# Optimization experiments

Hardware: AMD Instinct MI355X
Metric: run time of the kernel (lower is better)

## Reference

```python
import math
import jax, jax.numpy as jnp
import numpy as np

B, TP, E, H, HKV, D, M = 4, 8192, 4096, 32, 8, 128, 256
OUTLIERS = 8  # outlier_count_general
ROPE_THETA = 10000.0


def rotate_half(x):
    h = x.shape[-1] // 2
    return jnp.concatenate([-x[..., h:], x[..., :h]], axis=-1)


def setup_inputs() -> dict:
    key = jax.random.key(0)
    ks = jax.random.split(key, 9)
    hidden_states = jax.random.normal(ks[0], (B, 1, E), jnp.float32)
    # rotary embedding for the single new token at position TP
    inv_freq = 1.0 / (ROPE_THETA ** (np.arange(0, D, 2, dtype=np.float32) / D))
    ang = np.float32(TP) * inv_freq  # [D/2]
    cos = jnp.broadcast_to(jnp.asarray(np.concatenate([np.cos(ang), np.cos(ang)]), jnp.float32)[None, None, :], (B, 1, D))
    sin = jnp.broadcast_to(jnp.asarray(np.concatenate([np.sin(ang), np.sin(ang)]), jnp.float32)[None, None, :], (B, 1, D))
    past_keys = jax.random.normal(ks[1], (B, HKV, TP, D), jnp.float32)
    past_values = jax.random.normal(ks[2], (B, HKV, TP, D), jnp.float32)
    attention_mask = jnp.ones((B, TP + 1), jnp.float32)
    sc = E ** -0.5
    Wq = jax.random.normal(ks[3], (H * D, E), jnp.float32) * sc
    Wk = jax.random.normal(ks[4], (HKV * D, E), jnp.float32) * sc
    Wv = jax.random.normal(ks[5], (HKV * D, E), jnp.float32) * sc
    Wo = jax.random.normal(ks[6], (E, H * D), jnp.float32) * sc
    S_proj = jax.random.normal(ks[7], (D, M), jnp.float32)  # JL sketch matrix, shared across heads
    return {"hidden_states": hidden_states, "cos": cos, "sin": sin,
            "past_keys": past_keys, "past_values": past_values,
            "attention_mask": attention_mask,
            "Wq": Wq, "Wk": Wk, "Wv": Wv, "Wo": Wo, "S_proj": S_proj}


def reference(hidden_states, cos, sin, past_keys, past_values, attention_mask, Wq, Wk, Wv, Wo, S_proj):
    b = hidden_states.shape[0]
    d = past_keys.shape[-1]
    hkv = past_keys.shape[1]
    h = Wq.shape[0] // d
    g = h // hkv  # num_key_value_groups
    m = S_proj.shape[-1]

    # projections (decode step, q_len == 1)
    q = (hidden_states @ Wq.T).reshape(b, 1, h, d).transpose(0, 2, 1, 3)    # [b,H,1,d]
    k = (hidden_states @ Wk.T).reshape(b, 1, hkv, d).transpose(0, 2, 1, 3)  # [b,Hkv,1,d]
    v = (hidden_states @ Wv.T).reshape(b, 1, hkv, d).transpose(0, 2, 1, 3)

    # rotary
    c = cos[:, None, :, :]  # [b,1,1,d]
    s = sin[:, None, :, :]
    q = q * c + rotate_half(q) * s
    k = k * c + rotate_half(k) * s

    # update_sketch: append new key; keys held as raw values, quantized below
    keys = jnp.concatenate([past_keys, k], axis=2)      # [b,Hkv,T,d]
    values = jnp.concatenate([past_values, v], axis=2)  # [b,Hkv,T,d]

    # outlier channels: top-|.| channels per (batch, kv-head) kept exact
    ch_score = jnp.mean(jnp.abs(keys), axis=2)          # [b,Hkv,d]
    _, idx = jax.lax.top_k(ch_score, OUTLIERS)
    omask = jnp.sum(jax.nn.one_hot(idx, d, dtype=keys.dtype), axis=-2)  # [b,Hkv,d] in {0,1}

    # QJL 1-bit quantization of inlier part: store sign(S^T k_in) and ||k_in||
    k_in = keys * (1.0 - omask)[:, :, None, :]
    norms = jnp.linalg.norm(k_in, axis=-1)              # [b,Hkv,T]
    signs = jnp.sign(jnp.einsum('bktd,dm->bktm', k_in, S_proj))  # [b,Hkv,T,m]

    # attention_score: unbiased estimator q.k ~ ||k|| * sqrt(pi/2)/m * <S q, sign(S k)>
    qg = q[:, :, 0, :].reshape(b, hkv, g, d)            # group queries by kv head
    q_in = qg * (1.0 - omask)[:, :, None, :]
    q_out = qg * omask[:, :, None, :]
    qs = jnp.einsum('bkgd,dm->bkgm', q_in, S_proj)
    est = jnp.einsum('bkgm,bktm->bkgt', qs, signs) * (math.sqrt(math.pi / 2.0) / m) * norms[:, :, None, :]
    exact = jnp.einsum('bkgd,bktd->bkgt', q_out, keys)  # outlier channels kept full precision
    attn = (est + exact) / math.sqrt(d)                 # [b,Hkv,G,T]

    attn = attn + (1.0 - attention_mask)[:, None, None, :] * jnp.finfo(attn.dtype).min
    w = jax.nn.softmax(attn, axis=-1)

    out = jnp.einsum('bkgt,bktd->bkgd', w, values).reshape(b, 1, h * d)
    return out @ Wo.T  # [b,1,E]
```

## Files before the change

kernel.cpp:

```cpp
#include <hip/hip_runtime.h>
#include <math.h>

#define BB 4
#define TP 8192
#define TT 8193
#define EE 4096
#define HH 32
#define HKV 8
#define DD 128
#define MM 256
#define GG 4
#define NSEG 48
#define ESPLIT 4
#define TB 64
#define NT2 129
#define WCH 65

#define CJL 0.0048957583420918762f
#define RSQRT_D 0.08838834764831845f
#define NEG_HUGE -3.402823466e38f

#define KSTR 136
#define SSTR 276

typedef _Float16 f16x8 __attribute__((ext_vector_type(8)));
typedef _Float16 f16x4 __attribute__((ext_vector_type(4)));
typedef float f32x4 __attribute__((ext_vector_type(4)));

#define OFF_Q      0
#define OFF_KN     16384
#define OFF_VN     20480
#define OFF_MASKF  24576
#define OFF_QOV    28672
#define OFF_AO     29696
#define OFF_INT    46080
#define OFF_QSF    50432
#define OFF_SFRAG  115968
#define OFF_QKVP   181504
#define OFF_SCOREP 279808
#define OFF_LOGITS 541952

__global__ __launch_bounds__(256) void k1_kernel(
    const float* __restrict__ hs, const float* __restrict__ pk,
    const float* __restrict__ Wq, const float* __restrict__ Wk,
    const float* __restrict__ Wv, const float* __restrict__ Sp,
    float* __restrict__ qkvp, float* __restrict__ scorep,
    _Float16* __restrict__ Sfhi, _Float16* __restrict__ Sflo)
{
  __shared__ float shl[1024];
  __shared__ float sred[256];
  int bid = blockIdx.x, tid = threadIdx.x;
  if (bid < BB * NSEG * ESPLIT) {
    int c = bid & 3;
    int id = bid >> 2;
    int b = id / NSEG, seg = id % NSEG;
    const float* W;
    if (seg < HH)            W = Wq + (size_t)seg * DD * EE;
    else if (seg < HH + HKV) W = Wk + (size_t)(seg - HH) * DD * EE;
    else                     W = Wv + (size_t)(seg - HH - HKV) * DD * EE;
    for (int i = tid; i < 1024; i += 256) shl[i] = hs[b * EE + c * 1024 + i];
    __syncthreads();
    int row = tid & 127, half = tid >> 7;
    const float* wr = W + (size_t)row * EE + c * 1024 + half * 512;
    const float* hv = shl + half * 512;
    float acc = 0.f;
    for (int j = 0; j < 512; j += 4) {
      float4 w4 = *(const float4*)(wr + j);
      float4 h4 = *(const float4*)(hv + j);
      acc = fmaf(w4.x, h4.x, acc);
      acc = fmaf(w4.y, h4.y, acc);
      acc = fmaf(w4.z, h4.z, acc);
      acc = fmaf(w4.w, h4.w, acc);
    }
    sred[half * 128 + row] = acc;
    __syncthreads();
    if (tid < 128)
      qkvp[((size_t)(c * BB + b) * NSEG + seg) * DD + tid] = sred[tid] + sred[128 + tid];
  } else if (bid < BB * NSEG * ESPLIT + BB * HKV * 64) {
    int id = bid - BB * NSEG * ESPLIT;
    int chunk = id & 63, bk = id >> 6;
    const float* base = pk + (size_t)bk * TP * DD;
    int d = tid & 127, sub = tid >> 7;
    int t0 = chunk * 128;
    float acc = 0.f;
    for (int t = t0 + sub; t < t0 + 128; t += 2)
      acc += fabsf(base[(size_t)t * DD + d]);
    sred[sub * 128 + d] = acc;
    __syncthreads();
    if (tid < 128)
      scorep[((size_t)chunk * BB * HKV + bk) * DD + tid] = sred[tid] + sred[128 + tid];
  } else {
    int id = bid - BB * NSEG * ESPLIT - BB * HKV * 64;
    int mt = id >> 2, ks = id & 3;
    int w = tid >> 6, q = (tid >> 4) & 3, l15 = tid & 15;
    f16x8 hi, lo;
    #pragma unroll
    for (int j = 0; j < 8; ++j) {
      float s = Sp[(ks * 32 + q * 8 + j) * MM + w * 64 + mt * 16 + l15];
      _Float16 h = (_Float16)s;
      hi[j] = h;
      lo[j] = (_Float16)(s - (float)h);
    }
    *(f16x8*)&Sfhi[(size_t)(id * 256 + tid) * 8] = hi;
    *(f16x8*)&Sflo[(size_t)(id * 256 + tid) * 8] = lo;
  }
}

__global__ __launch_bounds__(256) void qkv_finalize_kernel(
    const float* __restrict__ qkvp, const float* __restrict__ cosb,
    const float* __restrict__ sinb, float* __restrict__ q_out,
    float* __restrict__ k_out, float* __restrict__ v_out)
{
  int gid = blockIdx.x * 256 + threadIdx.x;
  int b = gid / 6144;
  int r = gid - b * 6144;
  int seg = r >> 7, d = r & 127;
  float sum = 0.f;
  #pragma unroll
  for (int c = 0; c < 4; ++c)
    sum += qkvp[((size_t)(c * BB + b) * NSEG + seg) * DD + d];
  if (seg >= HH + HKV) {
    v_out[((size_t)b * HKV + (seg - HH - HKV)) * DD + d] = sum;
  } else {
    float part = 0.f;
    int dp = d ^ 64;
    #pragma unroll
    for (int c = 0; c < 4; ++c)
      part += qkvp[((size_t)(c * BB + b) * NSEG + seg) * DD + dp];
    float cc = cosb[b * DD + d], ss = sinb[b * DD + d];
    float other = (d < 64) ? -part : part;
    float rv = fmaf(sum, cc, other * ss);
    if (seg < HH) q_out[((size_t)b * HH + seg) * DD + d] = rv;
    else          k_out[((size_t)b * HKV + (seg - HH)) * DD + d] = rv;
  }
}

__global__ __launch_bounds__(128) void topk_kernel(
    const float* __restrict__ scorep, const float* __restrict__ k_new,
    float* __restrict__ maskf, int* __restrict__ pos, int* __restrict__ oidx)
{
  int bk = blockIdx.x;
  int tid = threadIdx.x;
  __shared__ float sv[DD];
  __shared__ int si[DD];
  float cur = 0.f;
  for (int c = 0; c < 64; ++c)
    cur += scorep[((size_t)c * BB * HKV + bk) * DD + tid];
  cur += fabsf(k_new[bk * DD + tid]);
  maskf[bk * DD + tid] = 1.f;
  pos[bk * DD + tid] = -1;
  for (int o = 0; o < 8; ++o) {
    sv[tid] = cur; si[tid] = tid;
    __syncthreads();
    for (int st = 64; st > 0; st >>= 1) {
      if (tid < st) {
        float a = sv[tid], c2 = sv[tid + st];
        int ia = si[tid], ic = si[tid + st];
        if (c2 > a || (c2 == a && ic < ia)) { sv[tid] = c2; si[tid] = ic; }
      }
      __syncthreads();
    }
    int mi = si[0];
    __syncthreads();
    if (tid == 0) oidx[bk * 8 + o] = mi;
    if (tid == mi) { pos[bk * DD + tid] = o; maskf[bk * DD + tid] = 0.f; cur = NEG_HUGE; }
  }
}

__global__ __launch_bounds__(256) void qs_kernel(
    const float* __restrict__ q_rope, const float* __restrict__ maskf,
    const float* __restrict__ Sp, const int* __restrict__ oidx,
    _Float16* __restrict__ qsfT, float* __restrict__ qoval)
{
  int bkg = blockIdx.x;
  int bk = bkg >> 2, g = bkg & 3;
  int b = bk >> 3, kv = bk & 7;
  __shared__ float qin[DD];
  __shared__ float qfull[DD];
  if (threadIdx.x < DD) {
    float qv = q_rope[((size_t)b * HH + kv * GG + g) * DD + threadIdx.x];
    qfull[threadIdx.x] = qv;
    qin[threadIdx.x] = qv * maskf[bk * DD + threadIdx.x];
  }
  __syncthreads();
  int m = threadIdx.x;
  float acc = 0.f;
  for (int d = 0; d < DD; ++d)
    acc = fmaf(qin[d], Sp[d * MM + m], acc);
  qsfT[((size_t)bk * 16 + g) * MM + m] = (_Float16)acc;
  if (g == 0) {
    #pragma unroll
    for (int n = 4; n < 16; ++n)
      qsfT[((size_t)bk * 16 + n) * MM + m] = (_Float16)0.f;
  }
  if (threadIdx.x < 8)
    qoval[bkg * 8 + threadIdx.x] = qfull[oidx[bk * 8 + threadIdx.x]];
}

__global__ __launch_bounds__(256) void logits_kernel(
    const float* __restrict__ pk, const float* __restrict__ k_new,
    const _Float16* __restrict__ Sfhi, const _Float16* __restrict__ Sflo,
    const _Float16* __restrict__ qsfT, const float* __restrict__ qoval,
    const int* __restrict__ pos, const float* __restrict__ amask,
    float* __restrict__ logits)
{
  __shared__ union {
    struct { _Float16 hi[TB * KSTR]; _Float16 lo[TB * KSTR]; } k;
    _Float16 ssg[TB * SSTR];
  } u;
  __shared__ float norm2[TB];
  __shared__ float koutl[TB][8];
  __shared__ float qovl[GG][8];

  int bk = blockIdx.x / NT2;
  int tile = blockIdx.x % NT2;
  int b = bk >> 3;
  int t0 = tile * TB;
  int tid = threadIdx.x;
  int l15 = tid & 15;
  int q   = (tid >> 4) & 3;
  int w   = tid >> 6;
  int mb  = w * 64;

  if (tid < 32) ((float*)qovl)[tid] = qoval[bk * 32 + tid];

  int d4 = (tid & 31) * 4;
  int p4[4];
  #pragma unroll
  for (int j = 0; j < 4; ++j) p4[j] = pos[bk * DD + d4 + j];

  #pragma unroll
  for (int iter = 0; iter < 8; ++iter) {
    int tl = iter * 8 + (tid >> 5);
    int tg = t0 + tl;
    float4 kv4 = make_float4(0.f, 0.f, 0.f, 0.f);
    if (tg < TP)       kv4 = *(const float4*)(pk + ((size_t)bk * TP + tg) * DD + d4);
    else if (tg == TP) kv4 = *(const float4*)(k_new + (size_t)bk * DD + d4);
    float vals[4] = {kv4.x, kv4.y, kv4.z, kv4.w};
    float nrm = 0.f;
    f16x4 hi4, lo4;
    #pragma unroll
    for (int j = 0; j < 4; ++j) {
      if (p4[j] >= 0) { koutl[tl][p4[j]] = vals[j]; vals[j] = 0.f; }
      nrm = fmaf(vals[j], vals[j], nrm);
      _Float16 h = (_Float16)vals[j];
      hi4[j] = h;
      lo4[j] = (_Float16)(vals[j] - (float)h);
    }
    *(f16x4*)&u.k.hi[tl * KSTR + d4] = hi4;
    *(f16x4*)&u.k.lo[tl * KSTR + d4] = lo4;
    #pragma unroll
    for (int off = 16; off > 0; off >>= 1) nrm += __shfl_xor(nrm, off);
    if ((tid & 31) == 0) norm2[tl] = nrm;
  }
  __syncthreads();

  f32x4 acc[4][4];
  #pragma unroll
  for (int ts = 0; ts < 4; ++ts)
    #pragma unroll
    for (int mt = 0; mt < 4; ++mt)
      acc[ts][mt] = (f32x4){0.f, 0.f, 0.f, 0.f};

  const f16x8* SH = (const f16x8*)Sfhi;
  const f16x8* SL = (const f16x8*)Sflo;
  #pragma unroll
  for (int ks = 0; ks < 4; ++ks) {
    f16x8 sh[4], sl[4], ah[4], al[4];
    #pragma unroll
    for (int mt = 0; mt < 4; ++mt) {
      sh[mt] = SH[(size_t)(mt * 4 + ks) * 256 + tid];
      sl[mt] = SL[(size_t)(mt * 4 + ks) * 256 + tid];
    }
    #pragma unroll
    for (int ts = 0; ts < 4; ++ts) {
      ah[ts] = *(const f16x8*)&u.k.hi[(ts * 16 + l15) * KSTR + ks * 32 + q * 8];
      al[ts] = *(const f16x8*)&u.k.lo[(ts * 16 + l15) * KSTR + ks * 32 + q * 8];
    }
    #pragma unroll
    for (int ts = 0; ts < 4; ++ts)
      #pragma unroll
      for (int mt = 0; mt < 4; ++mt) {
        acc[ts][mt] = __builtin_amdgcn_mfma_f32_16x16x32_f16(ah[ts], sh[mt], acc[ts][mt], 0, 0, 0);
        acc[ts][mt] = __builtin_amdgcn_mfma_f32_16x16x32_f16(al[ts], sh[mt], acc[ts][mt], 0, 0, 0);
        acc[ts][mt] = __builtin_amdgcn_mfma_f32_16x16x32_f16(ah[ts], sl[mt], acc[ts][mt], 0, 0, 0);
      }
  }
  __syncthreads();

  #pragma unroll
  for (int ts = 0; ts < 4; ++ts)
    #pragma unroll
    for (int mt = 0; mt < 4; ++mt)
      #pragma unroll
      for (int r = 0; r < 4; ++r) {
        int tl = ts * 16 + q * 4 + r;
        int mm = mb + mt * 16 + l15;
        u.ssg[tl * SSTR + mm] = acc[ts][mt][r] >= 0.f ? (_Float16)1.f : (_Float16)-1.f;
      }
  __syncthreads();

  f32x4 eacc = (f32x4){0.f, 0.f, 0.f, 0.f};
  const _Float16* qrow = qsfT + ((size_t)bk * 16 + l15) * MM;
  #pragma unroll
  for (int ks = 0; ks < 8; ++ks) {
    f16x8 as = *(const f16x8*)&u.ssg[(16 * w + l15) * SSTR + ks * 32 + q * 8];
    f16x8 bq = *(const f16x8*)&qrow[ks * 32 + q * 8];
    eacc = __builtin_amdgcn_mfma_f32_16x16x32_f16(as, bq, eacc, 0, 0, 0);
  }

  if (l15 < 4) {
    int g = l15;
    #pragma unroll
    for (int r = 0; r < 4; ++r) {
      int tl = 16 * w + q * 4 + r;
      int tg = t0 + tl;
      if (tg < TT) {
        float ex = 0.f;
        #pragma unroll
        for (int o = 0; o < 8; ++o) ex = fmaf(qovl[g][o], koutl[tl][o], ex);
        float logit = fmaf(eacc[r] * CJL, sqrtf(norm2[tl]), ex) * RSQRT_D;
        logit += (1.f - amask[b * TT + tg]) * NEG_HUGE;
        logits[((size_t)(bk * GG + g)) * TT + tg] = logit;
      }
    }
  }
}

__global__ __launch_bounds__(256) void softmax_kernel(
    float* __restrict__ logits, float* __restrict__ attn_o)
{
  int row = blockIdx.x;
  float* L = logits + (size_t)row * TT;
  int tid = threadIdx.x;
  int lane = tid & 63, wid = tid >> 6;
  __shared__ float red[8];
  if (tid < 128) attn_o[(size_t)row * DD + tid] = 0.f;
  float mx = NEG_HUGE;
  for (int i = tid; i < TT; i += 256) mx = fmaxf(mx, L[i]);
  #pragma unroll
  for (int off = 32; off > 0; off >>= 1) mx = fmaxf(mx, __shfl_xor(mx, off));
  if (lane == 0) red[wid] = mx;
  __syncthreads();
  if (tid == 0) red[4] = fmaxf(fmaxf(red[0], red[1]), fmaxf(red[2], red[3]));
  __syncthreads();
  mx = red[4];
  float sum = 0.f;
  for (int i = tid; i < TT; i += 256) sum += expf(L[i] - mx);
  #pragma unroll
  for (int off = 32; off > 0; off >>= 1) sum += __shfl_xor(sum, off);
  if (lane == 0) red[wid] = sum;
  __syncthreads();
  if (tid == 0) red[5] = (red[0] + red[1]) + (red[2] + red[3]);
  __syncthreads();
  float inv = 1.f / red[5];
  for (int i = tid; i < TT; i += 256) L[i] = expf(L[i] - mx) * inv;
}

__global__ __launch_bounds__(256) void wv_kernel(
    const float* __restrict__ pv, const float* __restrict__ v_new,
    const float* __restrict__ w, float* __restrict__ attn_out)
{
  __shared__ float red[8][GG][DD];
  int bk = blockIdx.x / WCH;
  int chunk = blockIdx.x % WCH;
  int b = bk >> 3, kv = bk & 7;
  int tsub = threadIdx.x >> 5;
  int d4 = (threadIdx.x & 31) * 4;
  int t0 = chunk * 128;
  int tend = (t0 + 128 < TT) ? t0 + 128 : TT;
  float4 acc[GG];
  #pragma unroll
  for (int g = 0; g < GG; ++g) acc[g] = make_float4(0.f, 0.f, 0.f, 0.f);
  const float* wbase = w + (size_t)bk * GG * TT;
  for (int t = t0 + tsub; t < tend; t += 8) {
    float4 v = (t < TP) ? *(const float4*)(pv + ((size_t)bk * TP + t) * DD + d4)
                        : *(const float4*)(v_new + (size_t)bk * DD + d4);
    #pragma unroll
    for (int g = 0; g < GG; ++g) {
      float wv = wbase[g * TT + t];
      acc[g].x = fmaf(wv, v.x, acc[g].x);
      acc[g].y = fmaf(wv, v.y, acc[g].y);
      acc[g].z = fmaf(wv, v.z, acc[g].z);
      acc[g].w = fmaf(wv, v.w, acc[g].w);
    }
  }
  #pragma unroll
  for (int g = 0; g < GG; ++g) *(float4*)&red[tsub][g][d4] = acc[g];
  __syncthreads();
  if (threadIdx.x < DD) {
    int d = threadIdx.x;
    #pragma unroll
    for (int g = 0; g < GG; ++g) {
      float s = 0.f;
      #pragma unroll
      for (int ts = 0; ts < 8; ++ts) s += red[ts][g][d];
      atomicAdd(&attn_out[((size_t)b * HH + kv * GG + g) * DD + d], s);
    }
  }
}

__global__ __launch_bounds__(256) void outproj_kernel(
    const float* __restrict__ attn_out, const float* __restrict__ Wo,
    float* __restrict__ out)
{
  __shared__ float al[EE];
  int b = blockIdx.x >> 7, seg = blockIdx.x & 127;
  int tid = threadIdx.x;
  for (int i = tid; i < EE; i += 256) al[i] = attn_out[(size_t)b * EE + i];
  __syncthreads();
  int rloc = tid >> 3, sub = tid & 7;
  int e = seg * 32 + rloc;
  const float* wr = Wo + (size_t)e * EE + sub * 512;
  const float* av = al + sub * 512;
  float acc = 0.f;
  for (int j = 0; j < 512; j += 4) {
    float4 w4 = *(const float4*)(wr + j);
    float4 a4 = *(const float4*)(av + j);
    acc = fmaf(w4.x, a4.x, acc);
    acc = fmaf(w4.y, a4.y, acc);
    acc = fmaf(w4.z, a4.z, acc);
    acc = fmaf(w4.w, a4.w, acc);
  }
  acc += __shfl_xor(acc, 1);
  acc += __shfl_xor(acc, 2);
  acc += __shfl_xor(acc, 4);
  if (sub == 0) out[(size_t)b * EE + e] = acc;
}

extern "C" void kernel_launch(void* const* d_in, const int* in_sizes, int n_in,
                              void* d_out, int out_size, void* d_ws, size_t ws_size,
                              hipStream_t stream)
{
  const float* hs    = (const float*)d_in[0];
  const float* cosb  = (const float*)d_in[1];
  const float* sinb  = (const float*)d_in[2];
  const float* pk    = (const float*)d_in[3];
  const float* pv    = (const float*)d_in[4];
  const float* amask = (const float*)d_in[5];
  const float* Wq    = (const float*)d_in[6];
  const float* Wk    = (const float*)d_in[7];
  const float* Wv    = (const float*)d_in[8];
  const float* Wo    = (const float*)d_in[9];
  const float* Sp    = (const float*)d_in[10];
  float* out = (float*)d_out;
  float* ws = (float*)d_ws;

  float* q_rope = ws + OFF_Q;
  float* k_new  = ws + OFF_KN;
  float* v_new  = ws + OFF_VN;
  float* maskf  = ws + OFF_MASKF;
  float* qoval  = ws + OFF_QOV;
  float* attn_o = ws + OFF_AO;
  int*   pos    = (int*)(ws + OFF_INT);
  int*   oidx   = pos + BB * HKV * DD;
  _Float16* qsfT = (_Float16*)(ws + OFF_QSF);
  _Float16* Sfhi = (_Float16*)(ws + OFF_SFRAG);
  _Float16* Sflo = Sfhi + 65536;
  float* qkvp   = ws + OFF_QKVP;
  float* scorep = ws + OFF_SCOREP;
  float* logits = ws + OFF_LOGITS;

  int k1_grid = BB * NSEG * ESPLIT + BB * HKV * 64 + 16;
  k1_kernel<<<k1_grid, 256, 0, stream>>>(hs, pk, Wq, Wk, Wv, Sp,
                                         qkvp, scorep, Sfhi, Sflo);
  qkv_finalize_kernel<<<96, 256, 0, stream>>>(qkvp, cosb, sinb,
                                              q_rope, k_new, v_new);
  topk_kernel<<<BB * HKV, 128, 0, stream>>>(scorep, k_new, maskf, pos, oidx);
  qs_kernel<<<BB * HKV * GG, 256, 0, stream>>>(q_rope, maskf, Sp, oidx, qsfT, qoval);
  logits_kernel<<<BB * HKV * NT2, 256, 0, stream>>>(pk, k_new, Sfhi, Sflo, qsfT,
                                                    qoval, pos, amask, logits);
  softmax_kernel<<<BB * HKV * GG, 256, 0, stream>>>(logits, attn_o);
  wv_kernel<<<BB * HKV * WCH, 256, 0, stream>>>(pv, v_new, logits, attn_o);
  outproj_kernel<<<BB * 128, 256, 0, stream>>>(attn_o, Wo, out);
}
```

Measured before the change: 583.4 us.

## Batch QKV and output projections across batch to read weights once

The QKV projection blocks now handle all four batch rows at once over half-width column slices, with twice the column splits. Each weight row is read from memory once instead of once per batch element, and the output projection applies the same batching. The pk abs-sum uses float4 loads, and wv_kernel stages the softmax weights in shared memory. The workspace layout is changed so logits overlap the qkvp region and scorep is moved; this relies on qkvp being dead before logits are written.

```diff
diff --git a/kernel.cpp b/kernel.cpp
--- a/kernel.cpp
+++ b/kernel.cpp
@@ -11,7 +11,7 @@
 #define MM 256
 #define GG 4
 #define NSEG 48
-#define ESPLIT 4
+#define ESPLIT 8
 #define TB 64
 #define NT2 129
 #define WCH 65
@@ -37,8 +37,11 @@
 #define OFF_QSF    50432
 #define OFF_SFRAG  115968
 #define OFF_QKVP   181504
-#define OFF_SCOREP 279808
-#define OFF_LOGITS 541952
+#define OFF_SCOREP 378112
+#define OFF_LOGITS 181504
+
+#define QKV_BLKS  (NSEG * ESPLIT)
+#define SCORE_BLKS (BB * HKV * 64)
 
 __global__ __launch_bounds__(256) void k1_kernel(
     const float* __restrict__ hs, const float* __restrict__ pk,
@@ -47,50 +50,67 @@
     float* __restrict__ qkvp, float* __restrict__ scorep,
     _Float16* __restrict__ Sfhi, _Float16* __restrict__ Sflo)
 {
-  __shared__ float shl[1024];
-  __shared__ float sred[256];
+  __shared__ float smem[3072];
   int bid = blockIdx.x, tid = threadIdx.x;
-  if (bid < BB * NSEG * ESPLIT) {
-    int c = bid & 3;
-    int id = bid >> 2;
-    int b = id / NSEG, seg = id % NSEG;
+  if (bid < QKV_BLKS) {
+    int c = bid & 7;
+    int seg = bid >> 3;
     const float* W;
     if (seg < HH)            W = Wq + (size_t)seg * DD * EE;
     else if (seg < HH + HKV) W = Wk + (size_t)(seg - HH) * DD * EE;
     else                     W = Wv + (size_t)(seg - HH - HKV) * DD * EE;
-    for (int i = tid; i < 1024; i += 256) shl[i] = hs[b * EE + c * 1024 + i];
+    float* hsl  = smem;
+    float* sred = smem + 2048;
+    for (int i = tid; i < 4 * 512; i += 256) {
+      int b = i >> 9, col = i & 511;
+      hsl[i] = hs[b * EE + c * 512 + col];
+    }
     __syncthreads();
     int row = tid & 127, half = tid >> 7;
-    const float* wr = W + (size_t)row * EE + c * 1024 + half * 512;
-    const float* hv = shl + half * 512;
-    float acc = 0.f;
-    for (int j = 0; j < 512; j += 4) {
+    const float* wr = W + (size_t)row * EE + c * 512 + half * 256;
+    float4 acc[BB];
+    #pragma unroll
+    for (int b = 0; b < BB; ++b) acc[b] = make_float4(0.f, 0.f, 0.f, 0.f);
+    for (int j = 0; j < 256; j += 4) {
       float4 w4 = *(const float4*)(wr + j);
-      float4 h4 = *(const float4*)(hv + j);
-      acc = fmaf(w4.x, h4.x, acc);
-      acc = fmaf(w4.y, h4.y, acc);
-      acc = fmaf(w4.z, h4.z, acc);
-      acc = fmaf(w4.w, h4.w, acc);
-    }
-    sred[half * 128 + row] = acc;
+      #pragma unroll
+      for (int b = 0; b < BB; ++b) {
+        float4 a4 = *(const float4*)&hsl[b * 512 + half * 256 + j];
+        acc[b].x = fmaf(w4.x, a4.x, acc[b].x);
+        acc[b].y = fmaf(w4.y, a4.y, acc[b].y);
+        acc[b].z = fmaf(w4.z, a4.z, acc[b].z);
+        acc[b].w = fmaf(w4.w, a4.w, acc[b].w);
+      }
+    }
+    #pragma unroll
+    for (int b = 0; b < BB; ++b)
+      sred[(half * BB + b) * DD + row] = (acc[b].x + acc[b].y) + (acc[b].z + acc[b].w);
     __syncthreads();
-    if (tid < 128)
-      qkvp[((size_t)(c * BB + b) * NSEG + seg) * DD + tid] = sred[tid] + sred[128 + tid];
-  } else if (bid < BB * NSEG * ESPLIT + BB * HKV * 64) {
-    int id = bid - BB * NSEG * ESPLIT;
+    for (int i = tid; i < BB * DD; i += 256) {
+      int b = i >> 7, d = i & 127;
+      qkvp[(((size_t)c * NSEG + seg) * BB + b) * DD + d] =
+          sred[b * DD + d] + sred[(BB + b) * DD + d];
+    }
+  } else if (bid < QKV_BLKS + SCORE_BLKS) {
+    int id = bid - QKV_BLKS;
     int chunk = id & 63, bk = id >> 6;
-    const float* base = pk + (size_t)bk * TP * DD;
-    int d = tid & 127, sub = tid >> 7;
-    int t0 = chunk * 128;
-    float acc = 0.f;
-    for (int t = t0 + sub; t < t0 + 128; t += 2)
-      acc += fabsf(base[(size_t)t * DD + d]);
-    sred[sub * 128 + d] = acc;
+    const float* base = pk + (size_t)bk * TP * DD + (size_t)chunk * 128 * DD;
+    int tsub = tid >> 5, d4 = (tid & 31) * 4;
+    float4 a = make_float4(0.f, 0.f, 0.f, 0.f);
+    for (int t = tsub; t < 128; t += 8) {
+      float4 v = *(const float4*)(base + (size_t)t * DD + d4);
+      a.x += fabsf(v.x); a.y += fabsf(v.y); a.z += fabsf(v.z); a.w += fabsf(v.w);
+    }
+    *(float4*)&smem[tsub * DD + d4] = a;
     __syncthreads();
-    if (tid < 128)
-      scorep[((size_t)chunk * BB * HKV + bk) * DD + tid] = sred[tid] + sred[128 + tid];
+    if (tid < DD) {
+      float s = 0.f;
+      #pragma unroll
+      for (int u = 0; u < 8; ++u) s += smem[u * DD + tid];
+      scorep[((size_t)chunk * BB * HKV + bk) * DD + tid] = s;
+    }
   } else {
-    int id = bid - BB * NSEG * ESPLIT - BB * HKV * 64;
+    int id = bid - QKV_BLKS - SCORE_BLKS;
     int mt = id >> 2, ks = id & 3;
     int w = tid >> 6, q = (tid >> 4) & 3, l15 = tid & 15;
     f16x8 hi, lo;
@@ -117,16 +137,16 @@
   int seg = r >> 7, d = r & 127;
   float sum = 0.f;
   #pragma unroll
-  for (int c = 0; c < 4; ++c)
-    sum += qkvp[((size_t)(c * BB + b) * NSEG + seg) * DD + d];
+  for (int c = 0; c < ESPLIT; ++c)
+    sum += qkvp[(((size_t)c * NSEG + seg) * BB + b) * DD + d];
   if (seg >= HH + HKV) {
     v_out[((size_t)b * HKV + (seg - HH - HKV)) * DD + d] = sum;
   } else {
     float part = 0.f;
     int dp = d ^ 64;
     #pragma unroll
-    for (int c = 0; c < 4; ++c)
-      part += qkvp[((size_t)(c * BB + b) * NSEG + seg) * DD + dp];
+    for (int c = 0; c < ESPLIT; ++c)
+      part += qkvp[(((size_t)c * NSEG + seg) * BB + b) * DD + dp];
     float cc = cosb[b * DD + d], ss = sinb[b * DD + d];
     float other = (d < 64) ? -part : part;
     float rv = fmaf(sum, cc, other * ss);
@@ -361,24 +381,31 @@
     const float* __restrict__ pv, const float* __restrict__ v_new,
     const float* __restrict__ w, float* __restrict__ attn_out)
 {
+  __shared__ float wl[GG * 128];
   __shared__ float red[8][GG][DD];
   int bk = blockIdx.x / WCH;
   int chunk = blockIdx.x % WCH;
   int b = bk >> 3, kv = bk & 7;
+  int t0 = chunk * 128;
+  const float* wbase = w + (size_t)bk * GG * TT;
+  for (int i = threadIdx.x; i < GG * 128; i += 256) {
+    int g = i >> 7, tloc = i & 127;
+    int t = t0 + tloc;
+    wl[i] = (t < TT) ? wbase[g * TT + t] : 0.f;
+  }
+  __syncthreads();
   int tsub = threadIdx.x >> 5;
   int d4 = (threadIdx.x & 31) * 4;
-  int t0 = chunk * 128;
   int tend = (t0 + 128 < TT) ? t0 + 128 : TT;
   float4 acc[GG];
   #pragma unroll
   for (int g = 0; g < GG; ++g) acc[g] = make_float4(0.f, 0.f, 0.f, 0.f);
-  const float* wbase = w + (size_t)bk * GG * TT;
   for (int t = t0 + tsub; t < tend; t += 8) {
     float4 v = (t < TP) ? *(const float4*)(pv + ((size_t)bk * TP + t) * DD + d4)
                         : *(const float4*)(v_new + (size_t)bk * DD + d4);
     #pragma unroll
     for (int g = 0; g < GG; ++g) {
-      float wv = wbase[g * TT + t];
+      float wv = wl[g * 128 + (t - t0)];
       acc[g].x = fmaf(wv, v.x, acc[g].x);
       acc[g].y = fmaf(wv, v.y, acc[g].y);
       acc[g].z = fmaf(wv, v.z, acc[g].z);
@@ -404,28 +431,41 @@
     const float* __restrict__ attn_out, const float* __restrict__ Wo,
     float* __restrict__ out)
 {
-  __shared__ float al[EE];
-  int b = blockIdx.x >> 7, seg = blockIdx.x & 127;
+  __shared__ float al[BB][16][260];
+  int seg = blockIdx.x;
   int tid = threadIdx.x;
-  for (int i = tid; i < EE; i += 256) al[i] = attn_out[(size_t)b * EE + i];
-  __syncthreads();
-  int rloc = tid >> 3, sub = tid & 7;
-  int e = seg * 32 + rloc;
-  const float* wr = Wo + (size_t)e * EE + sub * 512;
-  const float* av = al + sub * 512;
-  float acc = 0.f;
-  for (int j = 0; j < 512; j += 4) {
+  for (int i = tid; i < BB * EE; i += 256) {
+    int b = i >> 12, col = i & 4095;
+    al[b][col >> 8][col & 255] = attn_out[(size_t)b * EE + col];
+  }
+  __syncthreads();
+  int rloc = tid >> 4, sub = tid & 15;
+  int e = seg * 16 + rloc;
+  const float* wr = Wo + (size_t)e * EE + sub * 256;
+  float acc[BB] = {0.f, 0.f, 0.f, 0.f};
+  for (int j = 0; j < 256; j += 4) {
     float4 w4 = *(const float4*)(wr + j);
-    float4 a4 = *(const float4*)(av + j);
-    acc = fmaf(w4.x, a4.x, acc);
-    acc = fmaf(w4.y, a4.y, acc);
-    acc = fmaf(w4.z, a4.z, acc);
-    acc = fmaf(w4.w, a4.w, acc);
-  }
-  acc += __shfl_xor(acc, 1);
-  acc += __shfl_xor(acc, 2);
-  acc += __shfl_xor(acc, 4);
-  if (sub == 0) out[(size_t)b * EE + e] = acc;
+    #pragma unroll
+    for (int b = 0; b < BB; ++b) {
+      float4 a4 = *(const float4*)&al[b][sub][j];
+      acc[b] = fmaf(w4.x, a4.x, acc[b]);
+      acc[b] = fmaf(w4.y, a4.y, acc[b]);
+      acc[b] = fmaf(w4.z, a4.z, acc[b]);
+      acc[b] = fmaf(w4.w, a4.w, acc[b]);
+    }
+  }
+  #pragma unroll
+  for (int b = 0; b < BB; ++b) {
+    acc[b] += __shfl_xor(acc[b], 1);
+    acc[b] += __shfl_xor(acc[b], 2);
+    acc[b] += __shfl_xor(acc[b], 4);
+    acc[b] += __shfl_xor(acc[b], 8);
+  }
+  if (sub == 0) {
+    #pragma unroll
+    for (int b = 0; b < BB; ++b)
+      out[(size_t)b * EE + e] = acc[b];
+  }
 }
 
 extern "C" void kernel_launch(void* const* d_in, const int* in_sizes, int n_in,
@@ -461,7 +501,7 @@
   float* scorep = ws + OFF_SCOREP;
   float* logits = ws + OFF_LOGITS;
 
-  int k1_grid = BB * NSEG * ESPLIT + BB * HKV * 64 + 16;
+  int k1_grid = QKV_BLKS + SCORE_BLKS + 16;
   k1_kernel<<<k1_grid, 256, 0, stream>>>(hs, pk, Wq, Wk, Wv, Sp,
                                          qkvp, scorep, Sfhi, Sflo);
   qkv_finalize_kernel<<<96, 256, 0, stream>>>(qkvp, cosb, sinb,
@@ -472,5 +512,5 @@
                                                     qoval, pos, amask, logits);
   softmax_kernel<<<BB * HKV * GG, 256, 0, stream>>>(logits, attn_o);
   wv_kernel<<<BB * HKV * WCH, 256, 0, stream>>>(pv, v_new, logits, attn_o);
-  outproj_kernel<<<BB * 128, 256, 0, stream>>>(attn_o, Wo, out);
-}
+  outproj_kernel<<<256, 256, 0, stream>>>(attn_o, Wo, out);
+}
```

New measurement: 540.8 us. 7.3% less time.
